# Performance work log

Hardware: AMD Instinct MI355X
Metric: run time of the kernel (lower is better)

Reference implementation:

```python
import jax, jax.numpy as jnp
import numpy as np

ALPHA = 0.2          # LeakyReLU negative slope
N = 4096             # num nodes
E = 262144           # num edges (avg degree 64)
NFEAT = 512
NHID = 64
NHEAD = 8
NCLASS = 16
NEG_INF = -1e20


def setup_inputs() -> dict:
    key = jax.random.key(0)
    ks = jax.random.split(key, 8)
    features = jax.random.normal(ks[0], (N, NFEAT), dtype=jnp.float32)
    edge_list = jax.random.randint(ks[1], (2, E), 0, N, dtype=jnp.int64)
    # xavier-uniform-ish init scaled like gain=1.414
    W_heads = jax.random.normal(ks[2], (NHEAD, NFEAT, NHID), dtype=jnp.float32) * (1.414 / np.sqrt(NFEAT))
    a_heads = jax.random.normal(ks[3], (NHEAD, 2 * NHID, 1), dtype=jnp.float32) * 0.1
    b_heads = jnp.zeros((NHEAD, NHID), dtype=jnp.float32)
    W_out = jax.random.normal(ks[4], (NHEAD * NHID, NCLASS), dtype=jnp.float32) * (1.414 / np.sqrt(NHEAD * NHID))
    a_out = jax.random.normal(ks[5], (2 * NCLASS, 1), dtype=jnp.float32) * 0.1
    b_out = jnp.zeros((NCLASS,), dtype=jnp.float32)
    return {
        "features": features, "edge_list": edge_list,
        "W_heads": W_heads, "a_heads": a_heads, "b_heads": b_heads,
        "W_out": W_out, "a_out": a_out, "b_out": b_out,
    }


def _gatconv(x, src, tgt, W, a, b):
    # dropout layers are identity in eval mode
    h = x @ W                                             # [N, F_out]
    # edge scores: gather endpoints, concat, project, LeakyReLU
    a_input = jnp.concatenate([h[src], h[tgt]], axis=1)   # [E, 2*F_out]
    e = jax.nn.leaky_relu((a_input @ a)[:, 0], ALPHA)     # [E]
    n = h.shape[0]
    # dense NxN attention: -1e20 default, edge scores scattered in
    att = jnp.full((n, n), NEG_INF, dtype=h.dtype).at[src, tgt].set(e)
    att = jax.nn.softmax(att, axis=1)                     # rows w/o edges -> uniform (matches torch)
    return att @ h + b                                    # [N, F_out]


def reference(features, edge_list, W_heads, a_heads, b_heads, W_out, a_out, b_out):
    src, tgt = edge_list[0], edge_list[1]
    # multi-head GATConv, heads vmapped over stacked params -> [H, N, NHID]
    heads = jax.vmap(lambda W, a, b: _gatconv(features, src, tgt, W, a, b))(
        W_heads, a_heads, b_heads)
    # torch.cat over heads on dim=1 == transpose+reshape
    x = jnp.transpose(heads, (1, 0, 2)).reshape(N, NHEAD * NHID)
    x = jax.nn.elu(x)
    out = _gatconv(x, src, tgt, W_out, a_out, b_out)      # [N, NCLASS]
    return jax.nn.log_softmax(out, axis=1)
```

## Files before the change

### kernel.cpp

```cpp
#include <hip/hip_runtime.h>
#include <hip/hip_bf16.h>

#define NN 4096
#define NFEAT 512
#define NHID 64
#define NHEAD 8
#define NCLASS 16
#define CAP 192
#define LALPHA 0.2f

#define SZ2 (NHEAD*2*NHID)
#define SZ3 (NHEAD*NHID)
#define SZ4 (NFEAT*NCLASS)
#define SZ5 (2*NCLASS)
#define SZ6 (NCLASS)
#define NSMALL (SZ2+SZ3+SZ4+SZ5+SZ6)
#define NZERO (NN*NN/32 + NN + NHEAD*NHID + NCLASS)

typedef __attribute__((ext_vector_type(8))) short bf16x8;
typedef __attribute__((ext_vector_type(4))) float f32x4;
typedef __attribute__((ext_vector_type(8))) unsigned short u16x8;

__device__ __forceinline__ float b2f(unsigned short h) {
    return __uint_as_float(((unsigned int)h) << 16);
}
__device__ __forceinline__ unsigned short f2b(float f) {
    unsigned int u = __float_as_uint(f);
    unsigned int r = (u + 0x7fffu + ((u >> 16) & 1u)) >> 16;
    return (unsigned short)r;
}
__device__ __forceinline__ float waveMax(float v) {
#pragma unroll
    for (int m = 32; m >= 1; m >>= 1) v = fmaxf(v, __shfl_xor(v, m, 64));
    return v;
}
__device__ __forceinline__ float waveSum(float v) {
#pragma unroll
    for (int m = 32; m >= 1; m >>= 1) v += __shfl_xor(v, m, 64);
    return v;
}
__device__ __forceinline__ float lrelu(float e) {
    return e >= 0.f ? e : LALPHA * e;
}

__global__ void __launch_bounds__(256)
k_prep(const void* __restrict__ f, const void* __restrict__ Wh_,
       const void* __restrict__ ah_, const void* __restrict__ bh_,
       const void* __restrict__ Wo_, const void* __restrict__ ao_,
       const void* __restrict__ bo_, const int* __restrict__ e32,
       int E, int csb,
       unsigned short* __restrict__ featb,
       unsigned short* __restrict__ Wtb,
       float* __restrict__ smallf,
       unsigned int* __restrict__ bits) {
    __shared__ int sbf;
    int t = threadIdx.x;
    if (t < 64) {
        unsigned int w = ((const unsigned int*)f)[t];
        unsigned int lo = w & 0xffffu, e = (lo >> 7) & 0xffu;
        unsigned long long bal = __ballot(lo == 0u || (e >= 100u && e <= 140u));
        if (t == 0) sbf = (__popcll(bal) >= 40);
    }
    __syncthreads();
    bool bf = (sbf != 0);
    if (blockIdx.x < 128) {
        __shared__ float tile[64][33];
        int h = blockIdx.x >> 4, k0 = (blockIdx.x & 15) * 32;
        int n = t & 63, kh = t >> 6;
#pragma unroll
        for (int i = 0; i < 8; ++i) {
            int kk = kh * 8 + i;
            int si = (h << 15) + (k0 + kk) * NHID + n;
            float v = bf ? b2f(((const unsigned short*)Wh_)[si])
                         : ((const float*)Wh_)[si];
            tile[n][kk] = v;
        }
        __syncthreads();
        int n2 = t >> 2, kk0 = (t & 3) * 8;
        u16x8 o;
#pragma unroll
        for (int i = 0; i < 8; ++i) o[i] = f2b(tile[n2][kk0 + i]);
        *(u16x8*)&Wtb[(size_t)((h << 6) + n2) * NFEAT + k0 + kk0] = o;
    } else if ((int)blockIdx.x < 128 + csb) {
        __shared__ int s64f;
        if (t < 64) {
            unsigned long long bal = __ballot(e32[2 * t + 1] == 0);
            if (t == 0) s64f = (__popcll(bal) >= 48);
        }
        __syncthreads();
        int i = (blockIdx.x - 128) * 256 + t;
        if (i < E) {
            int s, tt;
            if (s64f) { s = e32[2 * i]; tt = e32[2 * (E + i)]; }
            else      { s = e32[i];     tt = e32[E + i]; }
            s &= (NN - 1); tt &= (NN - 1);
            unsigned int pos = (unsigned int)s * NN + (unsigned int)tt;
            atomicOr(&bits[pos >> 5], 1u << (pos & 31u));
        }
    } else {
        const int NF8 = NN * NFEAT / 8;
        int i = (blockIdx.x - 128 - csb) * 256 + t;
        int stride = (gridDim.x - 128 - csb) * 256;
        const int TOT = NF8 + NSMALL;
        for (; i < TOT; i += stride) {
            if (i < NF8) {
                if (bf) {
                    *(u16x8*)&featb[i * 8] = ((const u16x8*)f)[i];
                } else {
                    float4 lo = ((const float4*)f)[i * 2];
                    float4 hi = ((const float4*)f)[i * 2 + 1];
                    u16x8 o;
                    o[0] = f2b(lo.x); o[1] = f2b(lo.y); o[2] = f2b(lo.z); o[3] = f2b(lo.w);
                    o[4] = f2b(hi.x); o[5] = f2b(hi.y); o[6] = f2b(hi.z); o[7] = f2b(hi.w);
                    *(u16x8*)&featb[i * 8] = o;
                }
            } else {
                int r = i - NF8;
                const void* sp; int off;
                if (r < SZ2)                        { sp = ah_; off = r; }
                else if (r < SZ2 + SZ3)             { sp = bh_; off = r - SZ2; }
                else if (r < SZ2 + SZ3 + SZ4)       { sp = Wo_; off = r - SZ2 - SZ3; }
                else if (r < SZ2 + SZ3 + SZ4 + SZ5) { sp = ao_; off = r - SZ2 - SZ3 - SZ4; }
                else                                { sp = bo_; off = r - SZ2 - SZ3 - SZ4 - SZ5; }
                smallf[r] = bf ? b2f(((const unsigned short*)sp)[off])
                               : ((const float*)sp)[off];
            }
        }
    }
}

__global__ void __launch_bounds__(256)
k_gemm_ext(const unsigned short* __restrict__ Ab,
           const unsigned short* __restrict__ Wtb,
           const float* __restrict__ ah,
           unsigned short* __restrict__ Hb,
           float* __restrict__ s1, float* __restrict__ s2,
           float* __restrict__ cm1,
           const unsigned int* __restrict__ bits,
           int* __restrict__ deg, int* __restrict__ csr) {
    int t = threadIdx.x;
    if (blockIdx.x >= 256) {
        int wid = t >> 6, lane = t & 63;
        int n = (blockIdx.x - 256) * 4 + wid;
        uint2 w = *(const uint2*)&bits[n * 128 + lane * 2];
        int c = __popc(w.x) + __popc(w.y);
        int incl = c;
#pragma unroll
        for (int off = 1; off < 64; off <<= 1) {
            int u = __shfl_up(incl, off, 64);
            if (lane >= off) incl += u;
        }
        int excl = incl - c;
        int total = __shfl(incl, 63, 64);
        if (lane == 0) deg[n] = total;
        int base = n * CAP;
        int tbase = lane * 64;
        unsigned int x = w.x;
        while (x) {
            int b = __ffs(x) - 1; x &= x - 1;
            if (excl < CAP) csr[base + excl] = tbase + b;
            ++excl;
        }
        unsigned int y = w.y;
        while (y) {
            int b = __ffs(y) - 1; y &= y - 1;
            if (excl < CAP) csr[base + excl] = tbase + 32 + b;
            ++excl;
        }
        return;
    }
    __shared__ float cms[64];
    if (t < 64) cms[t] = 0.f;
    __syncthreads();
    int w = t >> 6, l = t & 63;
    int quad = l >> 4, l16 = l & 15;
    int h = blockIdx.x >> 5;
    int m0 = (blockIdx.x & 31) * 128 + w * 32;
    f32x4 acc[2][4] = {};
    const unsigned short* a0p = Ab + (size_t)(m0 + l16) * NFEAT + quad * 8;
    const unsigned short* a1p = a0p + 16 * NFEAT;
    const unsigned short* bp  = Wtb + ((size_t)h << 15) + (size_t)l16 * NFEAT + quad * 8;
#pragma unroll 4
    for (int k0 = 0; k0 < NFEAT; k0 += 32) {
        bf16x8 a0 = *(const bf16x8*)(a0p + k0);
        bf16x8 a1 = *(const bf16x8*)(a1p + k0);
#pragma unroll
        for (int nt = 0; nt < 4; ++nt) {
            bf16x8 b = *(const bf16x8*)(bp + (size_t)nt * 16 * NFEAT + k0);
            acc[0][nt] = __builtin_amdgcn_mfma_f32_16x16x32_bf16(a0, b, acc[0][nt], 0, 0, 0);
            acc[1][nt] = __builtin_amdgcn_mfma_f32_16x16x32_bf16(a1, b, acc[1][nt], 0, 0, 0);
        }
    }
    const float* av = ah + h * 2 * NHID;
    float p1[2][4] = {}, p2[2][4] = {};
#pragma unroll
    for (int rh = 0; rh < 2; ++rh) {
#pragma unroll
        for (int nt = 0; nt < 4; ++nt) {
            int col = nt * 16 + l16;
            float av1 = av[col], av2 = av[NHID + col];
            float csum = 0.f;
#pragma unroll
            for (int r = 0; r < 4; ++r) {
                float v = acc[rh][nt][r];
                int row = m0 + rh * 16 + quad * 4 + r;
                Hb[((size_t)row << 9) + (h << 6) + col] = f2b(v);
                p1[rh][r] += v * av1;
                p2[rh][r] += v * av2;
                csum += v;
            }
            atomicAdd(&cms[col], csum);
        }
    }
#pragma unroll
    for (int m = 8; m >= 1; m >>= 1)
#pragma unroll
        for (int rh = 0; rh < 2; ++rh)
#pragma unroll
            for (int r = 0; r < 4; ++r) {
                p1[rh][r] += __shfl_xor(p1[rh][r], m, 64);
                p2[rh][r] += __shfl_xor(p2[rh][r], m, 64);
            }
    if (l16 == 0) {
#pragma unroll
        for (int rh = 0; rh < 2; ++rh)
#pragma unroll
            for (int r = 0; r < 4; ++r) {
                int row = m0 + rh * 16 + quad * 4 + r;
                s1[(h << 12) + row] = p1[rh][r];
                s2[(h << 12) + row] = p2[rh][r];
            }
    }
    __syncthreads();
    if (t < 64) atomicAdd(&cm1[h * NHID + t], cms[t]);
}

__global__ void __launch_bounds__(256)
k_attn1f(const int* __restrict__ deg, const int* __restrict__ csr,
         const float* __restrict__ s1, const float* __restrict__ s2,
         const unsigned short* __restrict__ Hb,
         const float* __restrict__ bh, const float* __restrict__ cm1,
         const float* __restrict__ Wo, const float* __restrict__ ao,
         float* __restrict__ out2, float* __restrict__ s1o,
         float* __restrict__ s2o, float* __restrict__ cm2) {
    __shared__ float sW[4][CAP * 8];
    __shared__ int   sT[4][CAP];
    __shared__ float xr[4][NFEAT];
    __shared__ float cms[NCLASS];
    int t = threadIdx.x;
    if (t < NCLASS) cms[t] = 0.f;
    __syncthreads();
    int wid = t >> 6, lane = t & 63;
    int n = blockIdx.x * 4 + wid;
    int h = lane >> 3, jslot = lane & 7;
    int d = min(deg[n], CAP);
    float acc[8] = {};
    float rden = 1.f;
    if (d > 0) {
        const int* row = csr + (size_t)n * CAP;
        const float* s2h = s2 + ((size_t)h << 12);
        float s1n = s1[(h << 12) + n];
        float mx = -1e30f;
        for (int jb = 0; jb < d; jb += 8) {
            int j = jb + jslot;
            int tt = (j < d) ? (row[j] & (NN - 1)) : 0;
            float e = (j < d) ? lrelu(s1n + s2h[tt]) : -1e30f;
            sW[wid][(j << 3) + h] = e;
            if (h == 0) sT[wid][j] = tt;
            mx = fmaxf(mx, e);
        }
        mx = fmaxf(mx, __shfl_xor(mx, 1, 64));
        mx = fmaxf(mx, __shfl_xor(mx, 2, 64));
        mx = fmaxf(mx, __shfl_xor(mx, 4, 64));
        float den = 0.f;
        for (int jb = 0; jb < d; jb += 8) {
            int j = jb + jslot;
            float e = sW[wid][(j << 3) + h];
            float w = __expf(e - mx);
            sW[wid][(j << 3) + h] = w;
            den += w;
        }
        den += __shfl_xor(den, 1, 64);
        den += __shfl_xor(den, 2, 64);
        den += __shfl_xor(den, 4, 64);
        rden = 1.f / den;
        const unsigned short* Hp = Hb + lane * 8;
        int j = 0;
#pragma unroll 2
        for (; j + 2 <= d; j += 2) {
            int t0 = sT[wid][j], t1 = sT[wid][j + 1];
            float w0 = sW[wid][(j << 3) + h];
            float w1 = sW[wid][((j + 1) << 3) + h];
            u16x8 v0 = *(const u16x8*)(Hp + ((size_t)t0 << 9));
            u16x8 v1 = *(const u16x8*)(Hp + ((size_t)t1 << 9));
#pragma unroll
            for (int i = 0; i < 8; ++i)
                acc[i] += w0 * b2f(v0[i]) + w1 * b2f(v1[i]);
        }
        if (j < d) {
            int t0 = sT[wid][j];
            float w0 = sW[wid][(j << 3) + h];
            u16x8 v0 = *(const u16x8*)(Hp + ((size_t)t0 << 9));
#pragma unroll
            for (int i = 0; i < 8; ++i) acc[i] += w0 * b2f(v0[i]);
        }
    }
    float o[8];
    if (d == 0) {
#pragma unroll
        for (int i = 0; i < 8; ++i) o[i] = cm1[lane * 8 + i] * (1.0f / NN);
    } else {
#pragma unroll
        for (int i = 0; i < 8; ++i) o[i] = acc[i] * rden;
    }
#pragma unroll
    for (int i = 0; i < 8; ++i) {
        float v = o[i] + bh[lane * 8 + i];
        o[i] = v > 0.f ? v : __expf(v) - 1.f;
    }
    *(float4*)&xr[wid][lane * 8]     = make_float4(o[0], o[1], o[2], o[3]);
    *(float4*)&xr[wid][lane * 8 + 4] = make_float4(o[4], o[5], o[6], o[7]);
    int c = lane & 15, sub = lane >> 4;
    const float* xp = &xr[wid][sub * 128];
    const float* wp = Wo + sub * 128 * NCLASS + c;
    float a2 = 0.f;
#pragma unroll 8
    for (int kk = 0; kk < 128; ++kk) a2 += xp[kk] * wp[kk * NCLASS];
    a2 += __shfl_xor(a2, 16, 64);
    a2 += __shfl_xor(a2, 32, 64);
    if (lane < 16) out2[n * NCLASS + c] = a2;
    float r1 = a2 * ao[c], r2 = a2 * ao[NCLASS + c];
#pragma unroll
    for (int m = 8; m >= 1; m >>= 1) {
        r1 += __shfl_xor(r1, m, 16);
        r2 += __shfl_xor(r2, m, 16);
    }
    if (lane == 0) { s1o[n] = r1; s2o[n] = r2; }
    if (lane < 16) atomicAdd(&cms[c], a2);
    __syncthreads();
    if (t < NCLASS) atomicAdd(&cm2[t], cms[t]);
}

__global__ void __launch_bounds__(256)
k_attn2(const int* __restrict__ deg, const int* __restrict__ csr,
        const float* __restrict__ s1o, const float* __restrict__ s2o,
        const float* __restrict__ out2, const float* __restrict__ bo,
        const float* __restrict__ cm2, float* __restrict__ outp) {
    __shared__ float2 wts[4][CAP];
    __shared__ float o2s[4][16];
    int wid = threadIdx.x >> 6, lane = threadIdx.x & 63;
    int n = blockIdx.x * 4 + wid;
    int c = lane & 15;
    int d = min(deg[n], CAP);
    float val;
    if (d == 0) {
        val = cm2[c] * (1.0f / NN);
    } else {
        float s1n = s1o[n];
        const int* row = csr + (size_t)n * CAP;
        int t0 = (lane < d)       ? (row[lane]       & (NN - 1)) : 0;
        int t1 = (lane + 64 < d)  ? (row[lane + 64]  & (NN - 1)) : 0;
        int t2 = (lane + 128 < d) ? (row[lane + 128] & (NN - 1)) : 0;
        float e0 = (lane < d)       ? lrelu(s1n + s2o[t0]) : -1e30f;
        float e1 = (lane + 64 < d)  ? lrelu(s1n + s2o[t1]) : -1e30f;
        float e2 = (lane + 128 < d) ? lrelu(s1n + s2o[t2]) : -1e30f;
        float m = waveMax(fmaxf(e0, fmaxf(e1, e2)));
        float w0 = (lane < d)       ? __expf(e0 - m) : 0.f;
        float w1 = (lane + 64 < d)  ? __expf(e1 - m) : 0.f;
        float w2 = (lane + 128 < d) ? __expf(e2 - m) : 0.f;
        float den = waveSum(w0 + w1 + w2);
        wts[wid][lane]       = make_float2(w0, __int_as_float(t0 << 4));
        wts[wid][lane + 64]  = make_float2(w1, __int_as_float(t1 << 4));
        wts[wid][lane + 128] = make_float2(w2, __int_as_float(t2 << 4));
        int g2 = lane >> 2, q = lane & 3;
        float a4[4] = {};
        for (int j = g2; j < d; j += 16) {
            float2 p = wts[wid][j];
            float4 v = *(const float4*)(out2 + __float_as_int(p.y) + q * 4);
            a4[0] += p.x * v.x; a4[1] += p.x * v.y;
            a4[2] += p.x * v.z; a4[3] += p.x * v.w;
        }
#pragma unroll
        for (int m2 = 4; m2 <= 32; m2 <<= 1)
#pragma unroll
            for (int i = 0; i < 4; ++i) a4[i] += __shfl_xor(a4[i], m2, 64);
        if (lane < 4)
            *(float4*)&o2s[wid][lane * 4] = make_float4(a4[0], a4[1], a4[2], a4[3]);
        val = o2s[wid][c] / den;
    }
    val += bo[c];
    float mx = val;
#pragma unroll
    for (int m = 8; m >= 1; m >>= 1) mx = fmaxf(mx, __shfl_xor(mx, m, 16));
    float se = __expf(val - mx);
#pragma unroll
    for (int m = 8; m >= 1; m >>= 1) se += __shfl_xor(se, m, 16);
    float res = val - mx - __logf(se);
    if (lane < 16) outp[n * NCLASS + lane] = res;
}

extern "C" void kernel_launch(void* const* d_in, const int* in_sizes, int n_in,
                              void* d_out, int out_size, void* d_ws, size_t ws_size,
                              hipStream_t stream) {
    const void* features = d_in[0];
    const int*  edges    = (const int*)d_in[1];
    const void* W_heads  = d_in[2];
    const void* a_heads  = d_in[3];
    const void* b_heads  = d_in[4];
    const void* W_out    = d_in[5];
    const void* a_out    = d_in[6];
    const void* b_out    = d_in[7];
    int E = in_sizes[1] / 2;

    unsigned int* bits = (unsigned int*)d_ws;
    int*   deg  = (int*)(bits + (NN * NN / 32));
    float* cm1  = (float*)(deg + NN);
    float* cm2  = cm1 + NHEAD * NHID;
    int*   csr  = (int*)(cm2 + NCLASS);
    float* s1   = (float*)(csr + NN * CAP);
    float* s2   = s1 + NHEAD * NN;
    float* out2 = s2 + NHEAD * NN;
    float* s1o  = out2 + NN * NCLASS;
    float* s2o  = s1o + NN;
    unsigned short* Hb    = (unsigned short*)(s2o + NN);
    unsigned short* featb = Hb + (size_t)NHEAD * NN * NHID;
    unsigned short* Wtb   = featb + (size_t)NN * NFEAT;
    float* smallf = (float*)(Wtb + NHEAD * NHID * NFEAT);
    float* ahf = smallf;
    float* bhf = ahf + SZ2;
    float* Wof = bhf + SZ3;
    float* aof = Wof + SZ4;
    float* bof = aof + SZ5;
    float* outp = (float*)d_out;

    int csb = (E + 255) / 256;
    hipMemsetAsync(d_ws, 0, (size_t)NZERO * 4, stream);
    hipLaunchKernelGGL(k_prep, dim3(128 + csb + 896), dim3(256), 0, stream,
                       features, W_heads, a_heads, b_heads, W_out, a_out, b_out,
                       edges, E, csb, featb, Wtb, smallf, bits);
    hipLaunchKernelGGL(k_gemm_ext, dim3(256 + NN / 4), dim3(256), 0, stream,
                       featb, Wtb, ahf, Hb, s1, s2, cm1, bits, deg, csr);
    hipLaunchKernelGGL(k_attn1f, dim3(NN / 4), dim3(256), 0, stream,
                       deg, csr, s1, s2, Hb, bhf, cm1, Wof, aof, out2, s1o, s2o, cm2);
    hipLaunchKernelGGL(k_attn2, dim3(NN / 4), dim3(256), 0, stream,
                       deg, csr, s1o, s2o, out2, bof, cm2, outp);
}
```

Measured before the change: 147.3 us.

## Fuse all stages into one cooperative persistent kernel with grid syncs

Replaces the memset plus four separate kernel launches with a single cooperative kernel. Its phases (zeroing and prep, CSR build plus MFMA GEMM, layer-1 attention, layer-2 attention) are separated by grid-wide syncs, and each phase loops over virtual blocks. This is meant to remove launch overhead and inter-kernel idle gaps. It also drops redundant index masking and simplifies the shared-memory weight layout in the second attention stage. In exchange it pays for grid barriers, is limited by the co-resident block count, and falls back to the old multi-kernel path if the cooperative launch fails.

```diff
diff --git a/kernel.cpp b/kernel.cpp
--- a/kernel.cpp
+++ b/kernel.cpp
@@ -1,5 +1,8 @@
 #include <hip/hip_runtime.h>
 #include <hip/hip_bf16.h>
+#include <hip/hip_cooperative_groups.h>
+
+namespace cg = cooperative_groups;
 
 #define NN 4096
 #define NFEAT 512
@@ -41,6 +44,365 @@
 }
 __device__ __forceinline__ float lrelu(float e) {
     return e >= 0.f ? e : LALPHA * e;
+}
+
+__global__ void __launch_bounds__(256, 4)
+k_fused(const void* __restrict__ f, const void* __restrict__ Wh_,
+        const void* __restrict__ ah_, const void* __restrict__ bh_,
+        const void* __restrict__ Wo_, const void* __restrict__ ao_,
+        const void* __restrict__ bo_, const int* __restrict__ e32,
+        int E, int csb,
+        unsigned short* __restrict__ featb, unsigned short* __restrict__ Wtb,
+        float* __restrict__ smallf, unsigned int* __restrict__ bits,
+        int* __restrict__ deg, int* __restrict__ csr,
+        float* __restrict__ cm1, float* __restrict__ cm2,
+        float* __restrict__ s1, float* __restrict__ s2,
+        float* __restrict__ out2, float* __restrict__ s1o, float* __restrict__ s2o,
+        unsigned short* __restrict__ Hb, float* __restrict__ outp)
+{
+    cg::grid_group grid = cg::this_grid();
+    __shared__ __align__(16) char Bc[27712];
+    __shared__ int sbf, s64f;
+    int t = threadIdx.x, bid = blockIdx.x, nblk = gridDim.x;
+    int wid = t >> 6, lane = t & 63;
+
+    for (int i = bid * 256 + t; i < NZERO; i += nblk * 256) bits[i] = 0u;
+    if (t < 64) {
+        unsigned int w = ((const unsigned int*)f)[t];
+        unsigned int lo = w & 0xffffu, e = (lo >> 7) & 0xffu;
+        unsigned long long bal = __ballot(lo == 0u || (e >= 100u && e <= 140u));
+        if (t == 0) sbf = (__popcll(bal) >= 40);
+        unsigned long long bal2 = __ballot(e32[2 * t + 1] == 0);
+        if (t == 0) s64f = (__popcll(bal2) >= 48);
+    }
+    __threadfence();
+    grid.sync();
+    bool bf = (sbf != 0);
+
+    int NVB0 = 128 + csb + 896;
+    for (int vb = bid; vb < NVB0; vb += nblk) {
+        if (vb < 128) {
+            float (*tile)[33] = (float(*)[33])Bc;
+            int h = vb >> 4, k0 = (vb & 15) * 32;
+            int nn = t & 63, kh = t >> 6;
+#pragma unroll
+            for (int i = 0; i < 8; ++i) {
+                int kk = kh * 8 + i;
+                int si = (h << 15) + (k0 + kk) * NHID + nn;
+                float v = bf ? b2f(((const unsigned short*)Wh_)[si])
+                             : ((const float*)Wh_)[si];
+                tile[nn][kk] = v;
+            }
+            __syncthreads();
+            int n2 = t >> 2, kk0 = (t & 3) * 8;
+            u16x8 o;
+#pragma unroll
+            for (int i = 0; i < 8; ++i) o[i] = f2b(tile[n2][kk0 + i]);
+            *(u16x8*)&Wtb[(size_t)((h << 6) + n2) * NFEAT + k0 + kk0] = o;
+            __syncthreads();
+        } else if (vb < 128 + csb) {
+            int i = (vb - 128) * 256 + t;
+            if (i < E) {
+                int s, tt;
+                if (s64f) { s = e32[2 * i]; tt = e32[2 * (E + i)]; }
+                else      { s = e32[i];     tt = e32[E + i]; }
+                s &= (NN - 1); tt &= (NN - 1);
+                unsigned int pos = (unsigned int)s * NN + (unsigned int)tt;
+                atomicOr(&bits[pos >> 5], 1u << (pos & 31u));
+            }
+        } else {
+            const int NF8 = NN * NFEAT / 8;
+            const int TOT = NF8 + NSMALL;
+            for (int i = (vb - 128 - csb) * 256 + t; i < TOT; i += 896 * 256) {
+                if (i < NF8) {
+                    if (bf) {
+                        *(u16x8*)&featb[i * 8] = ((const u16x8*)f)[i];
+                    } else {
+                        float4 lo = ((const float4*)f)[i * 2];
+                        float4 hi = ((const float4*)f)[i * 2 + 1];
+                        u16x8 o;
+                        o[0] = f2b(lo.x); o[1] = f2b(lo.y); o[2] = f2b(lo.z); o[3] = f2b(lo.w);
+                        o[4] = f2b(hi.x); o[5] = f2b(hi.y); o[6] = f2b(hi.z); o[7] = f2b(hi.w);
+                        *(u16x8*)&featb[i * 8] = o;
+                    }
+                } else {
+                    int r = i - NF8;
+                    const void* sp; int off;
+                    if (r < SZ2)                        { sp = ah_; off = r; }
+                    else if (r < SZ2 + SZ3)             { sp = bh_; off = r - SZ2; }
+                    else if (r < SZ2 + SZ3 + SZ4)       { sp = Wo_; off = r - SZ2 - SZ3; }
+                    else if (r < SZ2 + SZ3 + SZ4 + SZ5) { sp = ao_; off = r - SZ2 - SZ3 - SZ4; }
+                    else                                { sp = bo_; off = r - SZ2 - SZ3 - SZ4 - SZ5; }
+                    smallf[r] = bf ? b2f(((const unsigned short*)sp)[off])
+                                   : ((const float*)sp)[off];
+                }
+            }
+        }
+    }
+    __threadfence();
+    grid.sync();
+
+    for (int vb = bid; vb < 1024; vb += nblk) {
+        {
+            int n = vb * 4 + wid;
+            uint2 w2 = *(const uint2*)&bits[n * 128 + lane * 2];
+            int c = __popc(w2.x) + __popc(w2.y);
+            int incl = c;
+#pragma unroll
+            for (int off = 1; off < 64; off <<= 1) {
+                int u = __shfl_up(incl, off, 64);
+                if (lane >= off) incl += u;
+            }
+            int excl = incl - c;
+            int total = __shfl(incl, 63, 64);
+            if (lane == 0) deg[n] = total;
+            int base = n * CAP;
+            int tbase = lane * 64;
+            unsigned int x = w2.x;
+            while (x) {
+                int b = __ffs(x) - 1; x &= x - 1;
+                if (excl < CAP) csr[base + excl] = tbase + b;
+                ++excl;
+            }
+            unsigned int y = w2.y;
+            while (y) {
+                int b = __ffs(y) - 1; y &= y - 1;
+                if (excl < CAP) csr[base + excl] = tbase + 32 + b;
+                ++excl;
+            }
+        }
+        {
+            float* sp1   = (float*)Bc;
+            float* sp2   = sp1 + 32;
+            float* cms64 = sp2 + 32;
+            if (t < 32) sp1[t] = 0.f;
+            else if (t < 64) sp2[t - 32] = 0.f;
+            __syncthreads();
+            int h = vb >> 7, m0 = (vb & 127) << 5;
+            int quad = lane >> 4, l16 = lane & 15;
+            f32x4 acc0 = {}, acc1 = {};
+            const unsigned short* a0p = featb + (size_t)(m0 + l16) * NFEAT + quad * 8;
+            const unsigned short* a1p = a0p + 16 * NFEAT;
+            const unsigned short* bp  = Wtb + ((size_t)h << 15) + (size_t)(wid * 16 + l16) * NFEAT + quad * 8;
+#pragma unroll 4
+            for (int k0 = 0; k0 < NFEAT; k0 += 32) {
+                bf16x8 a0 = *(const bf16x8*)(a0p + k0);
+                bf16x8 a1 = *(const bf16x8*)(a1p + k0);
+                bf16x8 b  = *(const bf16x8*)(bp + k0);
+                acc0 = __builtin_amdgcn_mfma_f32_16x16x32_bf16(a0, b, acc0, 0, 0, 0);
+                acc1 = __builtin_amdgcn_mfma_f32_16x16x32_bf16(a1, b, acc1, 0, 0, 0);
+            }
+            const float* av = smallf + h * 2 * NHID;
+            int col = wid * 16 + l16;
+            float av1 = av[col], av2 = av[NHID + col];
+            float p1v[2][4], p2v[2][4];
+            float csum = 0.f;
+#pragma unroll
+            for (int rh = 0; rh < 2; ++rh)
+#pragma unroll
+                for (int r = 0; r < 4; ++r) {
+                    float v = rh ? acc1[r] : acc0[r];
+                    int row = m0 + rh * 16 + quad * 4 + r;
+                    Hb[((size_t)row << 9) + (h << 6) + col] = f2b(v);
+                    p1v[rh][r] = v * av1;
+                    p2v[rh][r] = v * av2;
+                    csum += v;
+                }
+#pragma unroll
+            for (int m = 8; m >= 1; m >>= 1)
+#pragma unroll
+                for (int rh = 0; rh < 2; ++rh)
+#pragma unroll
+                    for (int r = 0; r < 4; ++r) {
+                        p1v[rh][r] += __shfl_xor(p1v[rh][r], m, 64);
+                        p2v[rh][r] += __shfl_xor(p2v[rh][r], m, 64);
+                    }
+            if (l16 == 0) {
+#pragma unroll
+                for (int rh = 0; rh < 2; ++rh)
+#pragma unroll
+                    for (int r = 0; r < 4; ++r) {
+                        atomicAdd(&sp1[rh * 16 + quad * 4 + r], p1v[rh][r]);
+                        atomicAdd(&sp2[rh * 16 + quad * 4 + r], p2v[rh][r]);
+                    }
+            }
+            csum += __shfl_xor(csum, 16, 64);
+            csum += __shfl_xor(csum, 32, 64);
+            if (lane < 16) cms64[wid * 16 + lane] = csum;
+            __syncthreads();
+            if (t < 32) {
+                s1[(h << 12) + m0 + t] = sp1[t];
+                s2[(h << 12) + m0 + t] = sp2[t];
+            }
+            if (t < 64) atomicAdd(&cm1[h * NHID + t], cms64[t]);
+        }
+    }
+    __threadfence();
+    grid.sync();
+
+    {
+        float* sW   = (float*)Bc;
+        int*   sTl  = (int*)(Bc + 24576);
+        float* cmsL = (float*)(Bc + 27648);
+        if (t < NCLASS) cmsL[t] = 0.f;
+        __syncthreads();
+        const float* bhf = smallf + SZ2;
+        const float* Wof = smallf + SZ2 + SZ3;
+        const float* aof = Wof + SZ4;
+        for (int vb = bid; vb < 1024; vb += nblk) {
+            int n = vb * 4 + wid;
+            int h = lane >> 3, jslot = lane & 7;
+            int d = min(deg[n], CAP);
+            float* sWw = sW + wid * (CAP * 8);
+            int*   sTw = sTl + wid * CAP;
+            const int* row = csr + (size_t)n * CAP;
+            float acc[8] = {};
+            float rden = 1.f;
+            if (d > 0) {
+                const float* s2h = s2 + ((size_t)h << 12);
+                float s1n = s1[(h << 12) + n];
+                float mx = -1e30f;
+                for (int jb = 0; jb < d; jb += 8) {
+                    int j = jb + jslot;
+                    int tt = (j < d) ? row[j] : 0;
+                    float e = (j < d) ? lrelu(s1n + s2h[tt]) : -1e30f;
+                    sWw[(j << 3) + h] = e;
+                    if (h == 0) sTw[j] = tt;
+                    mx = fmaxf(mx, e);
+                }
+                mx = fmaxf(mx, __shfl_xor(mx, 1, 64));
+                mx = fmaxf(mx, __shfl_xor(mx, 2, 64));
+                mx = fmaxf(mx, __shfl_xor(mx, 4, 64));
+                float den = 0.f;
+                for (int jb = 0; jb < d; jb += 8) {
+                    int j = jb + jslot;
+                    float e = sWw[(j << 3) + h];
+                    float w = __expf(e - mx);
+                    sWw[(j << 3) + h] = w;
+                    den += w;
+                }
+                den += __shfl_xor(den, 1, 64);
+                den += __shfl_xor(den, 2, 64);
+                den += __shfl_xor(den, 4, 64);
+                rden = 1.f / den;
+                const unsigned short* Hp = Hb + lane * 8;
+                int j = 0;
+#pragma unroll 2
+                for (; j + 2 <= d; j += 2) {
+                    int t0 = sTw[j], t1 = sTw[j + 1];
+                    float w0 = sWw[(j << 3) + h];
+                    float w1 = sWw[((j + 1) << 3) + h];
+                    u16x8 v0 = *(const u16x8*)(Hp + ((size_t)t0 << 9));
+                    u16x8 v1 = *(const u16x8*)(Hp + ((size_t)t1 << 9));
+#pragma unroll
+                    for (int i = 0; i < 8; ++i)
+                        acc[i] += w0 * b2f(v0[i]) + w1 * b2f(v1[i]);
+                }
+                if (j < d) {
+                    int t0 = sTw[j];
+                    float w0 = sWw[(j << 3) + h];
+                    u16x8 v0 = *(const u16x8*)(Hp + ((size_t)t0 << 9));
+#pragma unroll
+                    for (int i = 0; i < 8; ++i) acc[i] += w0 * b2f(v0[i]);
+                }
+            }
+            float o[8];
+            if (d == 0) {
+#pragma unroll
+                for (int i = 0; i < 8; ++i) o[i] = cm1[lane * 8 + i] * (1.0f / NN);
+            } else {
+#pragma unroll
+                for (int i = 0; i < 8; ++i) o[i] = acc[i] * rden;
+            }
+#pragma unroll
+            for (int i = 0; i < 8; ++i) {
+                float v = o[i] + bhf[lane * 8 + i];
+                o[i] = v > 0.f ? v : __expf(v) - 1.f;
+            }
+            float* xw = sWw;
+            *(float4*)&xw[lane * 8]     = make_float4(o[0], o[1], o[2], o[3]);
+            *(float4*)&xw[lane * 8 + 4] = make_float4(o[4], o[5], o[6], o[7]);
+            int c = lane & 15, sub = lane >> 4;
+            const float* xp = xw + sub * 128;
+            const float* wp = Wof + sub * 128 * NCLASS + c;
+            float a2 = 0.f;
+#pragma unroll 8
+            for (int kk = 0; kk < 128; ++kk) a2 += xp[kk] * wp[kk * NCLASS];
+            a2 += __shfl_xor(a2, 16, 64);
+            a2 += __shfl_xor(a2, 32, 64);
+            if (lane < 16) out2[n * NCLASS + c] = a2;
+            float r1 = a2 * aof[c], r2 = a2 * aof[NCLASS + c];
+#pragma unroll
+            for (int m = 8; m >= 1; m >>= 1) {
+                r1 += __shfl_xor(r1, m, 16);
+                r2 += __shfl_xor(r2, m, 16);
+            }
+            if (lane == 0) { s1o[n] = r1; s2o[n] = r2; }
+            if (lane < 16) atomicAdd(&cmsL[c], a2);
+        }
+        __syncthreads();
+        if (t < NCLASS) atomicAdd(&cm2[t], cmsL[t]);
+    }
+    __threadfence();
+    grid.sync();
+
+    {
+        float* wv  = (float*)Bc;
+        float* o2s = (float*)(Bc + 3072);
+        const float* bof = smallf + SZ2 + SZ3 + SZ4 + SZ5;
+        for (int vb = bid; vb < 1024; vb += nblk) {
+            int n = vb * 4 + wid;
+            int c = lane & 15;
+            int d = min(deg[n], CAP);
+            float val;
+            if (d == 0) {
+                val = cm2[c] * (1.0f / NN);
+            } else {
+                float s1n = s1o[n];
+                const int* rowp = csr + (size_t)n * CAP;
+                float* wvw = wv + wid * CAP;
+                int t0 = (lane < d)       ? rowp[lane]       : 0;
+                int t1 = (lane + 64 < d)  ? rowp[lane + 64]  : 0;
+                int t2 = (lane + 128 < d) ? rowp[lane + 128] : 0;
+                float e0 = (lane < d)       ? lrelu(s1n + s2o[t0]) : -1e30f;
+                float e1 = (lane + 64 < d)  ? lrelu(s1n + s2o[t1]) : -1e30f;
+                float e2 = (lane + 128 < d) ? lrelu(s1n + s2o[t2]) : -1e30f;
+                float m = waveMax(fmaxf(e0, fmaxf(e1, e2)));
+                float w0 = (lane < d)       ? __expf(e0 - m) : 0.f;
+                float w1 = (lane + 64 < d)  ? __expf(e1 - m) : 0.f;
+                float w2 = (lane + 128 < d) ? __expf(e2 - m) : 0.f;
+                float den = waveSum(w0 + w1 + w2);
+                wvw[lane]       = w0;
+                wvw[lane + 64]  = w1;
+                wvw[lane + 128] = w2;
+                int g2 = lane >> 2, q = lane & 3;
+                float a4[4] = {};
+                for (int j = g2; j < d; j += 16) {
+                    float w = wvw[j];
+                    int tt = rowp[j];
+                    float4 v = *(const float4*)(out2 + tt * NCLASS + q * 4);
+                    a4[0] += w * v.x; a4[1] += w * v.y;
+                    a4[2] += w * v.z; a4[3] += w * v.w;
+                }
+#pragma unroll
+                for (int m2 = 4; m2 <= 32; m2 <<= 1)
+#pragma unroll
+                    for (int i = 0; i < 4; ++i) a4[i] += __shfl_xor(a4[i], m2, 64);
+                if (lane < 4)
+                    *(float4*)&o2s[wid * 16 + lane * 4] = make_float4(a4[0], a4[1], a4[2], a4[3]);
+                val = o2s[wid * 16 + c] / den;
+            }
+            val += bof[c];
+            float mx = val;
+#pragma unroll
+            for (int m = 8; m >= 1; m >>= 1) mx = fmaxf(mx, __shfl_xor(mx, m, 16));
+            float se = __expf(val - mx);
+#pragma unroll
+            for (int m = 8; m >= 1; m >>= 1) se += __shfl_xor(se, m, 16);
+            float res = val - mx - __logf(se);
+            if (lane < 16) outp[n * NCLASS + lane] = res;
+        }
+    }
 }
 
 __global__ void __launch_bounds__(256)
@@ -263,7 +625,7 @@
         float mx = -1e30f;
         for (int jb = 0; jb < d; jb += 8) {
             int j = jb + jslot;
-            int tt = (j < d) ? (row[j] & (NN - 1)) : 0;
+            int tt = (j < d) ? row[j] : 0;
             float e = (j < d) ? lrelu(s1n + s2h[tt]) : -1e30f;
             sW[wid][(j << 3) + h] = e;
             if (h == 0) sT[wid][j] = tt;
@@ -318,10 +680,11 @@
         float v = o[i] + bh[lane * 8 + i];
         o[i] = v > 0.f ? v : __expf(v) - 1.f;
     }
-    *(float4*)&xr[wid][lane * 8]     = make_float4(o[0], o[1], o[2], o[3]);
-    *(float4*)&xr[wid][lane * 8 + 4] = make_float4(o[4], o[5], o[6], o[7]);
+    float* xw = xr[wid];
+    *(float4*)&xw[lane * 8]     = make_float4(o[0], o[1], o[2], o[3]);
+    *(float4*)&xw[lane * 8 + 4] = make_float4(o[4], o[5], o[6], o[7]);
     int c = lane & 15, sub = lane >> 4;
-    const float* xp = &xr[wid][sub * 128];
+    const float* xp = xw + sub * 128;
     const float* wp = Wo + sub * 128 * NCLASS + c;
     float a2 = 0.f;
 #pragma unroll 8
@@ -346,7 +709,7 @@
         const float* __restrict__ s1o, const float* __restrict__ s2o,
         const float* __restrict__ out2, const float* __restrict__ bo,
         const float* __restrict__ cm2, float* __restrict__ outp) {
-    __shared__ float2 wts[4][CAP];
+    __shared__ float wv[4][CAP];
     __shared__ float o2s[4][16];
     int wid = threadIdx.x >> 6, lane = threadIdx.x & 63;
     int n = blockIdx.x * 4 + wid;
@@ -357,10 +720,10 @@
         val = cm2[c] * (1.0f / NN);
     } else {
         float s1n = s1o[n];
-        const int* row = csr + (size_t)n * CAP;
-        int t0 = (lane < d)       ? (row[lane]       & (NN - 1)) : 0;
-        int t1 = (lane + 64 < d)  ? (row[lane + 64]  & (NN - 1)) : 0;
-        int t2 = (lane + 128 < d) ? (row[lane + 128] & (NN - 1)) : 0;
+        const int* rowp = csr + (size_t)n * CAP;
+        int t0 = (lane < d)       ? rowp[lane]       : 0;
+        int t1 = (lane + 64 < d)  ? rowp[lane + 64]  : 0;
+        int t2 = (lane + 128 < d) ? rowp[lane + 128] : 0;
         float e0 = (lane < d)       ? lrelu(s1n + s2o[t0]) : -1e30f;
         float e1 = (lane + 64 < d)  ? lrelu(s1n + s2o[t1]) : -1e30f;
         float e2 = (lane + 128 < d) ? lrelu(s1n + s2o[t2]) : -1e30f;
@@ -369,16 +732,17 @@
         float w1 = (lane + 64 < d)  ? __expf(e1 - m) : 0.f;
         float w2 = (lane + 128 < d) ? __expf(e2 - m) : 0.f;
         float den = waveSum(w0 + w1 + w2);
-        wts[wid][lane]       = make_float2(w0, __int_as_float(t0 << 4));
-        wts[wid][lane + 64]  = make_float2(w1, __int_as_float(t1 << 4));
-        wts[wid][lane + 128] = make_float2(w2, __int_as_float(t2 << 4));
+        wv[wid][lane]       = w0;
+        wv[wid][lane + 64]  = w1;
+        wv[wid][lane + 128] = w2;
         int g2 = lane >> 2, q = lane & 3;
         float a4[4] = {};
         for (int j = g2; j < d; j += 16) {
-            float2 p = wts[wid][j];
-            float4 v = *(const float4*)(out2 + __float_as_int(p.y) + q * 4);
-            a4[0] += p.x * v.x; a4[1] += p.x * v.y;
-            a4[2] += p.x * v.z; a4[3] += p.x * v.w;
+            float w = wv[wid][j];
+            int tt = rowp[j];
+            float4 v = *(const float4*)(out2 + tt * NCLASS + q * 4);
+            a4[0] += w * v.x; a4[1] += w * v.y;
+            a4[2] += w * v.z; a4[3] += w * v.w;
         }
 #pragma unroll
         for (int m2 = 4; m2 <= 32; m2 <<= 1)
@@ -411,6 +775,7 @@
     const void* a_out    = d_in[6];
     const void* b_out    = d_in[7];
     int E = in_sizes[1] / 2;
+    int csb = (E + 255) / 256;
 
     unsigned int* bits = (unsigned int*)d_ws;
     int*   deg  = (int*)(bits + (NN * NN / 32));
@@ -422,26 +787,56 @@
     float* out2 = s2 + NHEAD * NN;
     float* s1o  = out2 + NN * NCLASS;
     float* s2o  = s1o + NN;
-    unsigned short* Hb    = (unsigned short*)(s2o + NN);
-    unsigned short* featb = Hb + (size_t)NHEAD * NN * NHID;
+    float* smallf = s2o + NN;
+    unsigned short* Hb    = (unsigned short*)(smallf + NSMALL);
+    unsigned short* featb = Hb + (size_t)NN * NHEAD * NHID;
     unsigned short* Wtb   = featb + (size_t)NN * NFEAT;
-    float* smallf = (float*)(Wtb + NHEAD * NHID * NFEAT);
-    float* ahf = smallf;
-    float* bhf = ahf + SZ2;
-    float* Wof = bhf + SZ3;
-    float* aof = Wof + SZ4;
-    float* bof = aof + SZ5;
     float* outp = (float*)d_out;
 
-    int csb = (E + 255) / 256;
-    hipMemsetAsync(d_ws, 0, (size_t)NZERO * 4, stream);
-    hipLaunchKernelGGL(k_prep, dim3(128 + csb + 896), dim3(256), 0, stream,
-                       features, W_heads, a_heads, b_heads, W_out, a_out, b_out,
-                       edges, E, csb, featb, Wtb, smallf, bits);
-    hipLaunchKernelGGL(k_gemm_ext, dim3(256 + NN / 4), dim3(256), 0, stream,
-                       featb, Wtb, ahf, Hb, s1, s2, cm1, bits, deg, csr);
-    hipLaunchKernelGGL(k_attn1f, dim3(NN / 4), dim3(256), 0, stream,
-                       deg, csr, s1, s2, Hb, bhf, cm1, Wof, aof, out2, s1o, s2o, cm2);
-    hipLaunchKernelGGL(k_attn2, dim3(NN / 4), dim3(256), 0, stream,
-                       deg, csr, s1o, s2o, out2, bof, cm2, outp);
-}
+    static int coop_blocks = -2;
+    if (coop_blocks == -2) {
+        int maxB = 0, ncu = 0, dev = 0;
+        if (hipOccupancyMaxActiveBlocksPerMultiprocessor(
+                &maxB, reinterpret_cast<const void*>(&k_fused), 256, 0) != hipSuccess)
+            maxB = 0;
+        (void)hipGetDevice(&dev);
+        if (hipDeviceGetAttribute(&ncu, hipDeviceAttributeMultiprocessorCount, dev)
+                != hipSuccess)
+            ncu = 0;
+        coop_blocks = (maxB > 0 && ncu > 0) ? maxB * ncu : 0;
+    }
+    int nblk = coop_blocks > 1024 ? 1024 : coop_blocks;
+
+    bool done = false;
+    if (nblk >= 256) {
+        void* args[] = {
+            (void*)&features, (void*)&W_heads, (void*)&a_heads, (void*)&b_heads,
+            (void*)&W_out, (void*)&a_out, (void*)&b_out, (void*)&edges,
+            (void*)&E, (void*)&csb,
+            (void*)&featb, (void*)&Wtb, (void*)&smallf, (void*)&bits,
+            (void*)&deg, (void*)&csr, (void*)&cm1, (void*)&cm2,
+            (void*)&s1, (void*)&s2, (void*)&out2, (void*)&s1o, (void*)&s2o,
+            (void*)&Hb, (void*)&outp
+        };
+        hipError_t err = hipLaunchCooperativeKernel((const void*)k_fused,
+                                                    dim3(nblk), dim3(256),
+                                                    args, 0, stream);
+        if (err == hipSuccess) done = true;
+        else (void)hipGetLastError();
+    }
+    if (!done) {
+        hipMemsetAsync(d_ws, 0, (size_t)NZERO * 4, stream);
+        hipLaunchKernelGGL(k_prep, dim3(128 + csb + 896), dim3(256), 0, stream,
+                           features, W_heads, a_heads, b_heads, W_out, a_out, b_out,
+                           edges, E, csb, featb, Wtb, smallf, bits);
+        hipLaunchKernelGGL(k_gemm_ext, dim3(256 + NN / 4), dim3(256), 0, stream,
+                           featb, Wtb, smallf, Hb, s1, s2, cm1, bits, deg, csr);
+        hipLaunchKernelGGL(k_attn1f, dim3(NN / 4), dim3(256), 0, stream,
+                           deg, csr, s1, s2, Hb, smallf + SZ2, cm1,
+                           smallf + SZ2 + SZ3, smallf + SZ2 + SZ3 + SZ4,
+                           out2, s1o, s2o, cm2);
+        hipLaunchKernelGGL(k_attn2, dim3(NN / 4), dim3(256), 0, stream,
+                           deg, csr, s1o, s2o, out2,
+                           smallf + SZ2 + SZ3 + SZ4 + SZ5, cm2, outp);
+    }
+}
```

After: 532.8 us. 3.62x slower.

## Merge CSR build into every GEMM block and split heads across waves

Applied to the files above, without the earlier changes.

The GEMM kernel no longer uses separate blocks for CSR construction. Each of the 1024 blocks now builds CSR rows for four nodes and then computes a 32-row by 16-column tile per wave, with per-head score partials reduced through shared-memory atomics. The first attention pass aggregates four neighbours per iteration instead of two, which gives more loads in flight. The second pass reads neighbour indices straight from the CSR row instead of packing them into shared memory. The layout is also reshuffled so the small parameters sit before the bf16 buffers, and the redundant index masking is dropped.

```diff
diff --git a/kernel.cpp b/kernel.cpp
--- a/kernel.cpp
+++ b/kernel.cpp
@@ -130,7 +130,7 @@
 }
 
 __global__ void __launch_bounds__(256)
-k_gemm_ext(const unsigned short* __restrict__ Ab,
+k_gemm1024(const unsigned short* __restrict__ featb,
            const unsigned short* __restrict__ Wtb,
            const float* __restrict__ ah,
            unsigned short* __restrict__ Hb,
@@ -138,12 +138,13 @@
            float* __restrict__ cm1,
            const unsigned int* __restrict__ bits,
            int* __restrict__ deg, int* __restrict__ csr) {
-    int t = threadIdx.x;
-    if (blockIdx.x >= 256) {
-        int wid = t >> 6, lane = t & 63;
-        int n = (blockIdx.x - 256) * 4 + wid;
-        uint2 w = *(const uint2*)&bits[n * 128 + lane * 2];
-        int c = __popc(w.x) + __popc(w.y);
+    __shared__ float sp1[32], sp2[32], cms64[64];
+    int t = threadIdx.x, bid = blockIdx.x;
+    int wid = t >> 6, lane = t & 63;
+    {
+        int n = bid * 4 + wid;
+        uint2 w2 = *(const uint2*)&bits[n * 128 + lane * 2];
+        int c = __popc(w2.x) + __popc(w2.y);
         int incl = c;
 #pragma unroll
         for (int off = 1; off < 64; off <<= 1) {
@@ -155,84 +156,79 @@
         if (lane == 0) deg[n] = total;
         int base = n * CAP;
         int tbase = lane * 64;
-        unsigned int x = w.x;
+        unsigned int x = w2.x;
         while (x) {
             int b = __ffs(x) - 1; x &= x - 1;
             if (excl < CAP) csr[base + excl] = tbase + b;
             ++excl;
         }
-        unsigned int y = w.y;
+        unsigned int y = w2.y;
         while (y) {
             int b = __ffs(y) - 1; y &= y - 1;
             if (excl < CAP) csr[base + excl] = tbase + 32 + b;
             ++excl;
         }
-        return;
-    }
-    __shared__ float cms[64];
-    if (t < 64) cms[t] = 0.f;
+    }
+    if (t < 32) sp1[t] = 0.f;
+    else if (t < 64) sp2[t - 32] = 0.f;
     __syncthreads();
-    int w = t >> 6, l = t & 63;
-    int quad = l >> 4, l16 = l & 15;
-    int h = blockIdx.x >> 5;
-    int m0 = (blockIdx.x & 31) * 128 + w * 32;
-    f32x4 acc[2][4] = {};
-    const unsigned short* a0p = Ab + (size_t)(m0 + l16) * NFEAT + quad * 8;
+    int h = bid >> 7, m0 = (bid & 127) << 5;
+    int quad = lane >> 4, l16 = lane & 15;
+    f32x4 acc0 = {}, acc1 = {};
+    const unsigned short* a0p = featb + (size_t)(m0 + l16) * NFEAT + quad * 8;
     const unsigned short* a1p = a0p + 16 * NFEAT;
-    const unsigned short* bp  = Wtb + ((size_t)h << 15) + (size_t)l16 * NFEAT + quad * 8;
+    const unsigned short* bp  = Wtb + ((size_t)h << 15) + (size_t)(wid * 16 + l16) * NFEAT + quad * 8;
 #pragma unroll 4
     for (int k0 = 0; k0 < NFEAT; k0 += 32) {
         bf16x8 a0 = *(const bf16x8*)(a0p + k0);
         bf16x8 a1 = *(const bf16x8*)(a1p + k0);
-#pragma unroll
-        for (int nt = 0; nt < 4; ++nt) {
-            bf16x8 b = *(const bf16x8*)(bp + (size_t)nt * 16 * NFEAT + k0);
-            acc[0][nt] = __builtin_amdgcn_mfma_f32_16x16x32_bf16(a0, b, acc[0][nt], 0, 0, 0);
-            acc[1][nt] = __builtin_amdgcn_mfma_f32_16x16x32_bf16(a1, b, acc[1][nt], 0, 0, 0);
-        }
+        bf16x8 b  = *(const bf16x8*)(bp + k0);
+        acc0 = __builtin_amdgcn_mfma_f32_16x16x32_bf16(a0, b, acc0, 0, 0, 0);
+        acc1 = __builtin_amdgcn_mfma_f32_16x16x32_bf16(a1, b, acc1, 0, 0, 0);
     }
     const float* av = ah + h * 2 * NHID;
-    float p1[2][4] = {}, p2[2][4] = {};
-#pragma unroll
-    for (int rh = 0; rh < 2; ++rh) {
-#pragma unroll
-        for (int nt = 0; nt < 4; ++nt) {
-            int col = nt * 16 + l16;
-            float av1 = av[col], av2 = av[NHID + col];
-            float csum = 0.f;
+    int col = wid * 16 + l16;
+    float av1 = av[col], av2 = av[NHID + col];
+    float p1v[2][4], p2v[2][4];
+    float csum = 0.f;
+#pragma unroll
+    for (int rh = 0; rh < 2; ++rh)
+#pragma unroll
+        for (int r = 0; r < 4; ++r) {
+            float v = rh ? acc1[r] : acc0[r];
+            int row = m0 + rh * 16 + quad * 4 + r;
+            Hb[((size_t)row << 9) + (h << 6) + col] = f2b(v);
+            p1v[rh][r] = v * av1;
+            p2v[rh][r] = v * av2;
+            csum += v;
+        }
+#pragma unroll
+    for (int m = 8; m >= 1; m >>= 1)
+#pragma unroll
+        for (int rh = 0; rh < 2; ++rh)
 #pragma unroll
             for (int r = 0; r < 4; ++r) {
-                float v = acc[rh][nt][r];
-                int row = m0 + rh * 16 + quad * 4 + r;
-                Hb[((size_t)row << 9) + (h << 6) + col] = f2b(v);
-                p1[rh][r] += v * av1;
-                p2[rh][r] += v * av2;
-                csum += v;
-            }
-            atomicAdd(&cms[col], csum);
-        }
-    }
-#pragma unroll
-    for (int m = 8; m >= 1; m >>= 1)
-#pragma unroll
-        for (int rh = 0; rh < 2; ++rh)
-#pragma unroll
-            for (int r = 0; r < 4; ++r) {
-                p1[rh][r] += __shfl_xor(p1[rh][r], m, 64);
-                p2[rh][r] += __shfl_xor(p2[rh][r], m, 64);
+                p1v[rh][r] += __shfl_xor(p1v[rh][r], m, 64);
+                p2v[rh][r] += __shfl_xor(p2v[rh][r], m, 64);
             }
     if (l16 == 0) {
 #pragma unroll
         for (int rh = 0; rh < 2; ++rh)
 #pragma unroll
             for (int r = 0; r < 4; ++r) {
-                int row = m0 + rh * 16 + quad * 4 + r;
-                s1[(h << 12) + row] = p1[rh][r];
-                s2[(h << 12) + row] = p2[rh][r];
+                atomicAdd(&sp1[rh * 16 + quad * 4 + r], p1v[rh][r]);
+                atomicAdd(&sp2[rh * 16 + quad * 4 + r], p2v[rh][r]);
             }
     }
+    csum += __shfl_xor(csum, 16, 64);
+    csum += __shfl_xor(csum, 32, 64);
+    if (lane < 16) cms64[wid * 16 + lane] = csum;
     __syncthreads();
-    if (t < 64) atomicAdd(&cm1[h * NHID + t], cms[t]);
+    if (t < 32) {
+        s1[(h << 12) + m0 + t] = sp1[t];
+        s2[(h << 12) + m0 + t] = sp2[t];
+    }
+    if (t < 64) atomicAdd(&cm1[h * NHID + t], cms64[t]);
 }
 
 __global__ void __launch_bounds__(256)
@@ -263,7 +259,7 @@
         float mx = -1e30f;
         for (int jb = 0; jb < d; jb += 8) {
             int j = jb + jslot;
-            int tt = (j < d) ? (row[j] & (NN - 1)) : 0;
+            int tt = (j < d) ? row[j] : 0;
             float e = (j < d) ? lrelu(s1n + s2h[tt]) : -1e30f;
             sW[wid][(j << 3) + h] = e;
             if (h == 0) sT[wid][j] = tt;
@@ -286,18 +282,23 @@
         rden = 1.f / den;
         const unsigned short* Hp = Hb + lane * 8;
         int j = 0;
-#pragma unroll 2
-        for (; j + 2 <= d; j += 2) {
-            int t0 = sT[wid][j], t1 = sT[wid][j + 1];
+        for (; j + 4 <= d; j += 4) {
+            int t0 = sT[wid][j],     t1 = sT[wid][j + 1];
+            int t2 = sT[wid][j + 2], t3 = sT[wid][j + 3];
             float w0 = sW[wid][(j << 3) + h];
             float w1 = sW[wid][((j + 1) << 3) + h];
+            float w2 = sW[wid][((j + 2) << 3) + h];
+            float w3 = sW[wid][((j + 3) << 3) + h];
             u16x8 v0 = *(const u16x8*)(Hp + ((size_t)t0 << 9));
             u16x8 v1 = *(const u16x8*)(Hp + ((size_t)t1 << 9));
+            u16x8 v2 = *(const u16x8*)(Hp + ((size_t)t2 << 9));
+            u16x8 v3 = *(const u16x8*)(Hp + ((size_t)t3 << 9));
 #pragma unroll
             for (int i = 0; i < 8; ++i)
-                acc[i] += w0 * b2f(v0[i]) + w1 * b2f(v1[i]);
-        }
-        if (j < d) {
+                acc[i] += w0 * b2f(v0[i]) + w1 * b2f(v1[i])
+                        + w2 * b2f(v2[i]) + w3 * b2f(v3[i]);
+        }
+        for (; j < d; ++j) {
             int t0 = sT[wid][j];
             float w0 = sW[wid][(j << 3) + h];
             u16x8 v0 = *(const u16x8*)(Hp + ((size_t)t0 << 9));
@@ -318,10 +319,11 @@
         float v = o[i] + bh[lane * 8 + i];
         o[i] = v > 0.f ? v : __expf(v) - 1.f;
     }
-    *(float4*)&xr[wid][lane * 8]     = make_float4(o[0], o[1], o[2], o[3]);
-    *(float4*)&xr[wid][lane * 8 + 4] = make_float4(o[4], o[5], o[6], o[7]);
+    float* xw = xr[wid];
+    *(float4*)&xw[lane * 8]     = make_float4(o[0], o[1], o[2], o[3]);
+    *(float4*)&xw[lane * 8 + 4] = make_float4(o[4], o[5], o[6], o[7]);
     int c = lane & 15, sub = lane >> 4;
-    const float* xp = &xr[wid][sub * 128];
+    const float* xp = xw + sub * 128;
     const float* wp = Wo + sub * 128 * NCLASS + c;
     float a2 = 0.f;
 #pragma unroll 8
@@ -346,7 +348,7 @@
         const float* __restrict__ s1o, const float* __restrict__ s2o,
         const float* __restrict__ out2, const float* __restrict__ bo,
         const float* __restrict__ cm2, float* __restrict__ outp) {
-    __shared__ float2 wts[4][CAP];
+    __shared__ float wv[4][CAP];
     __shared__ float o2s[4][16];
     int wid = threadIdx.x >> 6, lane = threadIdx.x & 63;
     int n = blockIdx.x * 4 + wid;
@@ -357,10 +359,10 @@
         val = cm2[c] * (1.0f / NN);
     } else {
         float s1n = s1o[n];
-        const int* row = csr + (size_t)n * CAP;
-        int t0 = (lane < d)       ? (row[lane]       & (NN - 1)) : 0;
-        int t1 = (lane + 64 < d)  ? (row[lane + 64]  & (NN - 1)) : 0;
-        int t2 = (lane + 128 < d) ? (row[lane + 128] & (NN - 1)) : 0;
+        const int* rowp = csr + (size_t)n * CAP;
+        int t0 = (lane < d)       ? rowp[lane]       : 0;
+        int t1 = (lane + 64 < d)  ? rowp[lane + 64]  : 0;
+        int t2 = (lane + 128 < d) ? rowp[lane + 128] : 0;
         float e0 = (lane < d)       ? lrelu(s1n + s2o[t0]) : -1e30f;
         float e1 = (lane + 64 < d)  ? lrelu(s1n + s2o[t1]) : -1e30f;
         float e2 = (lane + 128 < d) ? lrelu(s1n + s2o[t2]) : -1e30f;
@@ -369,16 +371,17 @@
         float w1 = (lane + 64 < d)  ? __expf(e1 - m) : 0.f;
         float w2 = (lane + 128 < d) ? __expf(e2 - m) : 0.f;
         float den = waveSum(w0 + w1 + w2);
-        wts[wid][lane]       = make_float2(w0, __int_as_float(t0 << 4));
-        wts[wid][lane + 64]  = make_float2(w1, __int_as_float(t1 << 4));
-        wts[wid][lane + 128] = make_float2(w2, __int_as_float(t2 << 4));
+        wv[wid][lane]       = w0;
+        wv[wid][lane + 64]  = w1;
+        wv[wid][lane + 128] = w2;
         int g2 = lane >> 2, q = lane & 3;
         float a4[4] = {};
         for (int j = g2; j < d; j += 16) {
-            float2 p = wts[wid][j];
-            float4 v = *(const float4*)(out2 + __float_as_int(p.y) + q * 4);
-            a4[0] += p.x * v.x; a4[1] += p.x * v.y;
-            a4[2] += p.x * v.z; a4[3] += p.x * v.w;
+            float w = wv[wid][j];
+            int tt = rowp[j];
+            float4 v = *(const float4*)(out2 + tt * NCLASS + q * 4);
+            a4[0] += w * v.x; a4[1] += w * v.y;
+            a4[2] += w * v.z; a4[3] += w * v.w;
         }
 #pragma unroll
         for (int m2 = 4; m2 <= 32; m2 <<= 1)
@@ -411,6 +414,7 @@
     const void* a_out    = d_in[6];
     const void* b_out    = d_in[7];
     int E = in_sizes[1] / 2;
+    int csb = (E + 255) / 256;
 
     unsigned int* bits = (unsigned int*)d_ws;
     int*   deg  = (int*)(bits + (NN * NN / 32));
@@ -422,26 +426,23 @@
     float* out2 = s2 + NHEAD * NN;
     float* s1o  = out2 + NN * NCLASS;
     float* s2o  = s1o + NN;
-    unsigned short* Hb    = (unsigned short*)(s2o + NN);
-    unsigned short* featb = Hb + (size_t)NHEAD * NN * NHID;
+    float* smallf = s2o + NN;
+    unsigned short* Hb    = (unsigned short*)(smallf + NSMALL);
+    unsigned short* featb = Hb + (size_t)NN * NHEAD * NHID;
     unsigned short* Wtb   = featb + (size_t)NN * NFEAT;
-    float* smallf = (float*)(Wtb + NHEAD * NHID * NFEAT);
-    float* ahf = smallf;
-    float* bhf = ahf + SZ2;
-    float* Wof = bhf + SZ3;
-    float* aof = Wof + SZ4;
-    float* bof = aof + SZ5;
     float* outp = (float*)d_out;
 
-    int csb = (E + 255) / 256;
     hipMemsetAsync(d_ws, 0, (size_t)NZERO * 4, stream);
     hipLaunchKernelGGL(k_prep, dim3(128 + csb + 896), dim3(256), 0, stream,
                        features, W_heads, a_heads, b_heads, W_out, a_out, b_out,
                        edges, E, csb, featb, Wtb, smallf, bits);
-    hipLaunchKernelGGL(k_gemm_ext, dim3(256 + NN / 4), dim3(256), 0, stream,
-                       featb, Wtb, ahf, Hb, s1, s2, cm1, bits, deg, csr);
+    hipLaunchKernelGGL(k_gemm1024, dim3(1024), dim3(256), 0, stream,
+                       featb, Wtb, smallf, Hb, s1, s2, cm1, bits, deg, csr);
     hipLaunchKernelGGL(k_attn1f, dim3(NN / 4), dim3(256), 0, stream,
-                       deg, csr, s1, s2, Hb, bhf, cm1, Wof, aof, out2, s1o, s2o, cm2);
+                       deg, csr, s1, s2, Hb, smallf + SZ2, cm1,
+                       smallf + SZ2 + SZ3, smallf + SZ2 + SZ3 + SZ4,
+                       out2, s1o, s2o, cm2);
     hipLaunchKernelGGL(k_attn2, dim3(NN / 4), dim3(256), 0, stream,
-                       deg, csr, s1o, s2o, out2, bof, cm2, outp);
-}
+                       deg, csr, s1o, s2o, out2,
+                       smallf + SZ2 + SZ3 + SZ4 + SZ5, cm2, outp);
+}
```

Measured after the change: 155.5 us. 1.06x slower.
